# Performance work log

Measured on AMD Instinct MI355X. Metric: run time of the kernel, lower is better.

## Reference

```python
import jax, jax.numpy as jnp
import numpy as np

B, T, F, H, L = 16384, 24, 7, 8, 4
DENSE = [T * H, 1024, 2048, 4]


def setup_inputs() -> dict:
    key = jax.random.key(0)
    d = {"x": jax.random.normal(jax.random.fold_in(key, 0), (B, T, F), jnp.float32)}
    k = 1
    s = 1.0 / np.sqrt(H)  # torch LSTM init bound
    for l in range(L):
        in_dim = F if l == 0 else H
        for name, shape in [("Wih", (4 * H, in_dim)), ("Whh", (4 * H, H)), ("bih", (4 * H,)), ("bhh", (4 * H,))]:
            d[f"{name}{l}"] = jax.random.uniform(jax.random.fold_in(key, k), shape, jnp.float32, -s, s)
            k += 1
    for i in range(1, len(DENSE)):
        si = 1.0 / np.sqrt(DENSE[i - 1])
        d[f"Wd{i}"] = jax.random.uniform(jax.random.fold_in(key, k), (DENSE[i], DENSE[i - 1]), jnp.float32, -si, si)
        k += 1
        d[f"bd{i}"] = jax.random.uniform(jax.random.fold_in(key, k), (DENSE[i],), jnp.float32, -si, si)
        k += 1
    return d


def _lstm_layer(xs, Wih, Whh, b):
    # xs: [T, B, in] -> ys: [T, B, H]; torch gate order i,f,g,o
    Hn = Whh.shape[1]
    h0 = jnp.zeros((xs.shape[1], Hn), xs.dtype)

    def step(carry, xt):
        h, c = carry
        z = xt @ Wih.T + h @ Whh.T + b  # [B, 4H]
        i, f, g, o = jnp.split(z, 4, axis=-1)
        c = jax.nn.sigmoid(f) * c + jax.nn.sigmoid(i) * jnp.tanh(g)
        h = jax.nn.sigmoid(o) * jnp.tanh(c)
        return (h, c), h

    (_, _), ys = jax.lax.scan(step, (h0, h0), xs)
    return ys


def _forward(x, lstm_params, dense_params):
    xs = jnp.transpose(x, (1, 0, 2))  # [T, B, F]
    for (Wih, Whh, bih, bhh) in lstm_params:
        xs = _lstm_layer(xs, Wih, Whh, bih + bhh)
    out = jnp.transpose(xs, (1, 0, 2)).reshape(x.shape[0], T * H)  # [B, 192]
    (W1, b1), (W2, b2), (W3, b3) = dense_params
    out = jax.nn.relu(out @ W1.T + b1)
    out = jax.nn.relu(out @ W2.T + b2)
    return out @ W3.T + b3  # [B, num_classes]


def reference(x, Wih0, Whh0, bih0, bhh0, Wih1, Whh1, bih1, bhh1, Wih2, Whh2, bih2, bhh2, Wih3, Whh3, bih3, bhh3, Wd1, bd1, Wd2, bd2, Wd3, bd3):
    lstm_params = [(Wih0, Whh0, bih0, bhh0), (Wih1, Whh1, bih1, bhh1), (Wih2, Whh2, bih2, bhh2), (Wih3, Whh3, bih3, bhh3)]
    dense_params = [(Wd1, bd1), (Wd2, bd2), (Wd3, bd3)]
    return _forward(x, lstm_params, dense_params)
```

## Files before the change

### kernel.cpp

```cpp
#include <hip/hip_runtime.h>
#include <hip/hip_bf16.h>

typedef __attribute__((ext_vector_type(4))) float f32x4;
typedef __attribute__((ext_vector_type(16))) float f32x16;
typedef __attribute__((ext_vector_type(2))) float f32x2;
typedef __attribute__((ext_vector_type(8))) short bf16x8;

__device__ __forceinline__ ushort f2bf(float f) {
    union { float f; uint u; } v; v.f = f;
    uint u = v.u;
    return (ushort)((u + 0x7fffu + ((u >> 16) & 1u)) >> 16);
}
__device__ __forceinline__ float sigm(float x) {
    return __builtin_amdgcn_rcpf(1.0f + __builtin_amdgcn_exp2f(x * -1.442695040888963f));
}
__device__ __forceinline__ float tanh_(float x) {
    return 2.0f * __builtin_amdgcn_rcpf(1.0f + __builtin_amdgcn_exp2f(x * -2.885390081777927f)) - 1.0f;
}
__device__ __forceinline__ uint pk2(float a, float b) {
    uint r; asm("v_cvt_pk_bf16_f32 %0, %1, %2" : "=v"(r) : "v"(a), "v"(b)); return r;
}
__device__ __forceinline__ bf16x8 pk8(f32x4 lo, f32x4 hi) {
    union { bf16x8 v; uint u[4]; } r;
    r.u[0] = pk2(lo[0], lo[1]); r.u[1] = pk2(lo[2], lo[3]);
    r.u[2] = pk2(hi[0], hi[1]); r.u[3] = pk2(hi[2], hi[3]);
    return r.v;
}

typedef const __attribute__((address_space(1))) unsigned int ga_u32;
typedef __attribute__((address_space(3))) unsigned int lds_u32;
__device__ __forceinline__ void g2l16(const void* g, void* l) {
    __builtin_amdgcn_global_load_lds((ga_u32*)(unsigned long long)g,
                                     (lds_u32*)(unsigned int)(unsigned long long)l,
                                     16, 0, 0);
}

struct LstmW {
    const float* wih[4];
    const float* whh[4];
    const float* bih[4];
    const float* bhh[4];
};

__device__ __forceinline__ void gates8p(const f32x2 w01[8], const f32x2 w23[8],
                                        const float xv8[8], f32x2& a01, f32x2& a23) {
#pragma unroll
    for (int k = 0; k < 8; ++k) {
        f32x2 xv = {xv8[k], xv8[k]};
        a01 += w01[k] * xv;
        a23 += w23[k] * xv;
    }
}
__device__ __forceinline__ void cellup(f32x2 a01, f32x2 a23, float& h, float& c) {
    c = sigm(a01.y) * c + sigm(a01.x) * tanh_(a23.x);
    h = sigm(a23.y) * tanh_(c);
}
__device__ __forceinline__ void ld8(const float* p, float v[8]) {
    float4 a = *(const float4*)p;
    float4 b = *(const float4*)(p + 4);
    v[0] = a.x; v[1] = a.y; v[2] = a.z; v[3] = a.w;
    v[4] = b.x; v[5] = b.y; v[6] = b.z; v[7] = b.w;
}

__global__ __launch_bounds__(256) void pre_kernel(const float* __restrict__ x, LstmW p,
                                                  const float* __restrict__ W1,
                                                  const float* __restrict__ b1,
                                                  const float* __restrict__ W2,
                                                  ushort* __restrict__ W2b,
                                                  const float* __restrict__ b3,
                                                  float* __restrict__ out,
                                                  ushort* __restrict__ H1) {
    const int tid = threadIdx.x;
    if (blockIdx.x >= 512) {
        const int tg = (blockIdx.x - 512) * 256 + tid;
        if (tg < 16384) {
            float4 bv = {b3[0], b3[1], b3[2], b3[3]};
            ((float4*)out)[tg] = bv;
        }
#pragma unroll
        for (int s = 0; s < 4; ++s) {
            int i = tg + s * 131072;
            float4 v = ((const float4*)W2)[i];
            ushort4 r; r.x = f2bf(v.x); r.y = f2bf(v.y); r.z = f2bf(v.z); r.w = f2bf(v.w);
            ((ushort4*)W2b)[i] = r;
        }
        return;
    }

    __shared__ float xs[32 * 168];
    __shared__ float hb[32 * 200];

    const int e0 = blockIdx.x * 32;
    {
        const float4* s = (const float4*)(x + (size_t)e0 * 168);
        float4* d = (float4*)xs;
        for (int i = tid; i < 1344; i += 256) d[i] = s[i];
    }
    __syncthreads();

    const int el = tid >> 3, j = tid & 7;
    float* hr = hb + el * 200;
    const float* xr = xs + el * 168;

    f32x2 wx01[8], wx23[8], wh01[8], wh23[8], b01, b23;

    {
        const float* Wih = p.wih[0];
        const float* Whh = p.whh[0];
#pragma unroll
        for (int k = 0; k < 7; ++k) {
            wx01[k] = {Wih[(0 + j) * 7 + k], Wih[(8 + j) * 7 + k]};
            wx23[k] = {Wih[(16 + j) * 7 + k], Wih[(24 + j) * 7 + k]};
        }
#pragma unroll
        for (int k = 0; k < 8; ++k) {
            wh01[k] = {Whh[(0 + j) * 8 + k], Whh[(8 + j) * 8 + k]};
            wh23[k] = {Whh[(16 + j) * 8 + k], Whh[(24 + j) * 8 + k]};
        }
        b01 = {p.bih[0][j] + p.bhh[0][j], p.bih[0][8 + j] + p.bhh[0][8 + j]};
        b23 = {p.bih[0][16 + j] + p.bhh[0][16 + j], p.bih[0][24 + j] + p.bhh[0][24 + j]};

        float h = 0.f, c = 0.f;
        {
            f32x2 a01 = b01, a23 = b23;
#pragma unroll
            for (int k = 0; k < 7; ++k) {
                f32x2 xv = {xr[k], xr[k]};
                a01 += wx01[k] * xv; a23 += wx23[k] * xv;
            }
            cellup(a01, a23, h, c);
            hr[j] = h;
        }
        for (int t = 1; t < 24; ++t) {
            f32x2 a01 = b01, a23 = b23;
#pragma unroll
            for (int k = 0; k < 7; ++k) {
                f32x2 xv = {xr[t * 7 + k], xr[t * 7 + k]};
                a01 += wx01[k] * xv; a23 += wx23[k] * xv;
            }
            float hp[8]; ld8(&hr[(t - 1) * 8], hp);
            gates8p(wh01, wh23, hp, a01, a23);
            cellup(a01, a23, h, c);
            hr[t * 8 + j] = h;
        }
    }

#pragma unroll
    for (int l = 1; l < 4; ++l) {
        const float* Wih = p.wih[l];
        const float* Whh = p.whh[l];
#pragma unroll
        for (int k = 0; k < 8; ++k) {
            wx01[k] = {Wih[(0 + j) * 8 + k], Wih[(8 + j) * 8 + k]};
            wx23[k] = {Wih[(16 + j) * 8 + k], Wih[(24 + j) * 8 + k]};
            wh01[k] = {Whh[(0 + j) * 8 + k], Whh[(8 + j) * 8 + k]};
            wh23[k] = {Whh[(16 + j) * 8 + k], Whh[(24 + j) * 8 + k]};
        }
        b01 = {p.bih[l][j] + p.bhh[l][j], p.bih[l][8 + j] + p.bhh[l][8 + j]};
        b23 = {p.bih[l][16 + j] + p.bhh[l][16 + j], p.bih[l][24 + j] + p.bhh[l][24 + j]};

        float h = 0.f, c = 0.f;
        {
            float xin[8]; ld8(&hr[0], xin);
            f32x2 a01 = b01, a23 = b23;
            gates8p(wx01, wx23, xin, a01, a23);
            cellup(a01, a23, h, c);
            hr[j] = h;
        }
        for (int t = 1; t < 24; ++t) {
            float xin[8]; ld8(&hr[t * 8], xin);
            float hp[8];  ld8(&hr[(t - 1) * 8], hp);
            f32x2 a01 = b01, a23 = b23;
            gates8p(wx01, wx23, xin, a01, a23);
            gates8p(wh01, wh23, hp, a01, a23);
            cellup(a01, a23, h, c);
            hr[t * 8 + j] = h;
        }
    }

    __syncthreads();
    {
        const int lane = tid & 63;
        const int wv = tid >> 6;
        const int l15 = lane & 15, kq = lane >> 4;
        const int nw0 = wv * 256;

        bf16x8 abf[2][6];
#pragma unroll
        for (int mf = 0; mf < 2; ++mf)
#pragma unroll
            for (int ks = 0; ks < 6; ++ks) {
                const float* ap = hb + (mf * 16 + l15) * 200 + ks * 32 + kq * 8;
                f32x4 lo = *(const f32x4*)ap;
                f32x4 hi = *(const f32x4*)(ap + 4);
                abf[mf][ks] = pk8(lo, hi);
            }
#pragma unroll
        for (int nf = 0; nf < 16; ++nf) {
            const int col = nw0 + nf * 16 + l15;
            const float* wrow = W1 + (size_t)col * 192;
            bf16x8 bbf[6];
#pragma unroll
            for (int ks = 0; ks < 6; ++ks) {
                f32x4 lo = *(const f32x4*)(wrow + ks * 32 + kq * 8);
                f32x4 hi = *(const f32x4*)(wrow + ks * 32 + kq * 8 + 4);
                bbf[ks] = pk8(lo, hi);
            }
            f32x4 a0 = {0.f, 0.f, 0.f, 0.f}, a1 = {0.f, 0.f, 0.f, 0.f};
#pragma unroll
            for (int ks = 0; ks < 6; ++ks) {
                a0 = __builtin_amdgcn_mfma_f32_16x16x32_bf16(abf[0][ks], bbf[ks], a0, 0, 0, 0);
                a1 = __builtin_amdgcn_mfma_f32_16x16x32_bf16(abf[1][ks], bbf[ks], a1, 0, 0, 0);
            }
            const float bv = b1[col];
#pragma unroll
            for (int r = 0; r < 4; ++r) {
                H1[(size_t)(e0 + kq * 4 + r) * 1024 + col]      = f2bf(fmaxf(a0[r] + bv, 0.f));
                H1[(size_t)(e0 + 16 + kq * 4 + r) * 1024 + col] = f2bf(fmaxf(a1[r] + bv, 0.f));
            }
        }
    }
}

template <int OFFB>
__device__ __forceinline__ bf16x8 dsr(unsigned a) {
    bf16x8 r;
    asm volatile("ds_read_b128 %0, %1 offset:%2"
                 : "=v"(r) : "v"(a), "i"(OFFB));
    return r;
}
template <int QA, int QB, int KS>
__device__ __forceinline__ void mma_sub(f32x4 acc[8][4], const bf16x8 afr[8],
                                        const bf16x8 br[4]) {
#pragma unroll
    for (int mi = 0; mi < 4; ++mi)
#pragma unroll
        for (int ni = 0; ni < 2; ++ni)
            acc[QA * 4 + mi][QB * 2 + ni] = __builtin_amdgcn_mfma_f32_16x16x32_bf16(
                afr[mi * 2 + KS], br[ni * 2 + KS], acc[QA * 4 + mi][QB * 2 + ni],
                0, 0, 0);
}

#define SBAR()  __builtin_amdgcn_s_barrier()
#define SCHED0() __builtin_amdgcn_sched_barrier(0)
#define LGKM(N) do { asm volatile("s_waitcnt lgkmcnt(" #N ")"); SCHED0(); } while (0)
#define VMC(N)  do { asm volatile("s_waitcnt vmcnt(" #N ")" ::: "memory"); } while (0)
#define PRIO1() __builtin_amdgcn_s_setprio(1)
#define PRIO0() do { __builtin_amdgcn_s_setprio(0); SCHED0(); } while (0)

__global__ __launch_bounds__(512) void gemm2_kernel(const ushort* __restrict__ A,
                                                    const ushort* __restrict__ W,
                                                    const float* __restrict__ bias,
                                                    const float* __restrict__ W3,
                                                    float* __restrict__ outf) {
    __shared__ alignas(16) ushort smem[65536];
    __shared__ alignas(16) float w3s[1040];

    const int tid = threadIdx.x;
    const int wg = ((int)blockIdx.x & 7) * 64 + ((int)blockIdx.x >> 3);
    const int m0 = (wg >> 3) << 8;
    const int n0 = (wg & 7) << 8;

    const int lane = tid & 63;
    const int wv = tid >> 6;

    const int lrow = tid >> 3;
    const int lc8 = ((tid & 7) ^ (lrow & 7)) << 3;
    const ushort* Ag = A + (size_t)(m0 + lrow) * 1024 + lc8;
    const ushort* Bg = W + (size_t)(n0 + lrow) * 1024 + lc8;
    ushort* const sA0 = smem;
    ushort* const sB0 = smem + 16384;
    ushort* const sA1 = smem + 32768;
    ushort* const sB1 = smem + 49152;
    const int srow64 = (wv << 3) * 64;

    const int l15 = lane & 15, kq = lane >> 4, r7 = l15 & 7;
    const int wM = wv >> 2, wN = wv & 3;
    const unsigned sbase = (unsigned)(unsigned long long)&smem[0];
    const unsigned pc0B = (unsigned)((kq ^ r7) << 4);
    const unsigned pc1B = pc0B ^ 64u;
    const unsigned aRowB = (unsigned)((wM * 128 + l15) * 128);
    const unsigned bRowB = (unsigned)((wN * 64 + l15) * 128);
    const unsigned aA0p0 = sbase + aRowB + pc0B;
    const unsigned aA0p1 = sbase + aRowB + pc1B;
    const unsigned aA1p0 = aA0p0 + 65536u;
    const unsigned aA1p1 = aA0p1 + 65536u;
    const unsigned bB0p0 = sbase + 32768u + bRowB + pc0B;
    const unsigned bB0p1 = sbase + 32768u + bRowB + pc1B;
    const unsigned bB1p0 = bB0p0 + 65536u;
    const unsigned bB1p1 = bB0p1 + 65536u;

    auto stA = [&](int buf, int h, int kt) {
        ushort* b = buf ? sA1 : sA0;
#pragma unroll
        for (int c = 0; c < 2; ++c)
            g2l16(Ag + (size_t)(h * 128 + c * 64) * 1024 + kt * 64,
                  b + (h * 128 + c * 64) * 64 + srow64);
    };
    auto stB = [&](int buf, int h, int kt) {
        ushort* b = buf ? sB1 : sB0;
#pragma unroll
        for (int c = 0; c < 2; ++c)
            g2l16(Bg + (size_t)(h * 128 + c * 64) * 1024 + kt * 64,
                  b + (h * 128 + c * 64) * 64 + srow64);
    };

    f32x4 acc[8][4];
#pragma unroll
    for (int i = 0; i < 8; ++i)
#pragma unroll
        for (int j = 0; j < 4; ++j)
#pragma unroll
            for (int r = 0; r < 4; ++r) acc[i][j][r] = 0.f;

#pragma unroll
    for (int i = 0; i < 2; ++i) {
        int idx = tid + i * 512;
        w3s[(idx >> 8) * 260 + (idx & 255)] = W3[(size_t)(idx >> 8) * 2048 + n0 + (idx & 255)];
    }
    float bias4[4];
#pragma unroll
    for (int ni = 0; ni < 4; ++ni) bias4[ni] = bias[n0 + wN * 64 + ni * 16 + l15];

    stA(0, 0, 0); stA(0, 1, 0); stB(0, 0, 0); stB(0, 1, 0);
    stB(1, 0, 1); stB(1, 1, 1); stA(1, 0, 1);
    asm volatile("s_waitcnt lgkmcnt(0)");
    VMC(6);
    SBAR(); SCHED0();

    bf16x8 afr[8], b0r[4], b1r[4];
    afr[0] = dsr<0>(aA0p0);    afr[2] = dsr<2048>(aA0p0);
    afr[4] = dsr<4096>(aA0p0); afr[6] = dsr<6144>(aA0p0);
    b0r[0] = dsr<0>(bB0p0);    b0r[2] = dsr<2048>(bB0p0);

#pragma unroll 1
    for (int it = 0; it < 8; ++it) {
        const int k1 = 2 * it + 1, k2 = 2 * it + 2, k3 = 2 * it + 3;
        const bool nl = (it < 7);
        SBAR(); SCHED0();
        afr[1] = dsr<0>(aA0p1);    afr[3] = dsr<2048>(aA0p1);
        afr[5] = dsr<4096>(aA0p1); afr[7] = dsr<6144>(aA0p1);
        b0r[1] = dsr<0>(bB0p1);    b0r[3] = dsr<2048>(bB0p1);
        stA(1, 1, k1);
        LGKM(6); PRIO1(); mma_sub<0, 0, 0>(acc, afr, b0r); PRIO0();
        b1r[0] = dsr<4096>(bB0p0); b1r[2] = dsr<6144>(bB0p0);
        LGKM(2); PRIO1(); mma_sub<0, 0, 1>(acc, afr, b0r); PRIO0();
        SBAR(); SCHED0();
        b1r[1] = dsr<4096>(bB0p1); b1r[3] = dsr<6144>(bB0p1);
        LGKM(2); PRIO1(); mma_sub<0, 1, 0>(acc, afr, b1r); PRIO0();
        afr[0] = dsr<8192>(aA0p0);  afr[2] = dsr<10240>(aA0p0);
        afr[4] = dsr<12288>(aA0p0); afr[6] = dsr<14336>(aA0p0);
        LGKM(4); PRIO1(); mma_sub<0, 1, 1>(acc, afr, b1r); PRIO0();
        SBAR(); SCHED0();
        afr[1] = dsr<8192>(aA0p1);  afr[3] = dsr<10240>(aA0p1);
        afr[5] = dsr<12288>(aA0p1); afr[7] = dsr<14336>(aA0p1);
        if (nl) stB(0, 0, k2);
        LGKM(4); PRIO1(); mma_sub<1, 1, 0>(acc, afr, b1r); PRIO0();
        LGKM(0); PRIO1(); mma_sub<1, 1, 1>(acc, afr, b1r); PRIO0();
        if (nl) { VMC(2); } else { VMC(0); }
        SBAR(); SCHED0();
        if (nl) { stB(0, 1, k2); stA(0, 0, k2); }
        PRIO1(); mma_sub<1, 0, 0>(acc, afr, b0r); PRIO0();
        afr[0] = dsr<8192>(aA1p0);  afr[2] = dsr<10240>(aA1p0);
        afr[4] = dsr<12288>(aA1p0); afr[6] = dsr<14336>(aA1p0);
        b0r[0] = dsr<0>(bB1p0);     b0r[2] = dsr<2048>(bB1p0);
        PRIO1(); mma_sub<1, 0, 1>(acc, afr, b0r); PRIO0();
        SBAR(); SCHED0();
        afr[1] = dsr<8192>(aA1p1);  afr[3] = dsr<10240>(aA1p1);
        afr[5] = dsr<12288>(aA1p1); afr[7] = dsr<14336>(aA1p1);
        b0r[1] = dsr<0>(bB1p1);     b0r[3] = dsr<2048>(bB1p1);
        if (nl) stA(0, 1, k2);
        LGKM(6); PRIO1(); mma_sub<1, 0, 0>(acc, afr, b0r); PRIO0();
        b1r[0] = dsr<4096>(bB1p0); b1r[2] = dsr<6144>(bB1p0);
        LGKM(2); PRIO1(); mma_sub<1, 0, 1>(acc, afr, b0r); PRIO0();
        SBAR(); SCHED0();
        b1r[1] = dsr<4096>(bB1p1); b1r[3] = dsr<6144>(bB1p1);
        LGKM(2); PRIO1(); mma_sub<1, 1, 0>(acc, afr, b1r); PRIO0();
        afr[0] = dsr<0>(aA1p0);    afr[2] = dsr<2048>(aA1p0);
        afr[4] = dsr<4096>(aA1p0); afr[6] = dsr<6144>(aA1p0);
        LGKM(4); PRIO1(); mma_sub<1, 1, 1>(acc, afr, b1r); PRIO0();
        SBAR(); SCHED0();
        afr[1] = dsr<0>(aA1p1);    afr[3] = dsr<2048>(aA1p1);
        afr[5] = dsr<4096>(aA1p1); afr[7] = dsr<6144>(aA1p1);
        if (nl) stB(1, 0, k3);
        LGKM(4); PRIO1(); mma_sub<0, 1, 0>(acc, afr, b1r); PRIO0();
        LGKM(0); PRIO1(); mma_sub<0, 1, 1>(acc, afr, b1r); PRIO0();
        if (nl) { VMC(2); }
        SBAR(); SCHED0();
        if (nl) { stB(1, 1, k3); stA(1, 0, k3); }
        PRIO1(); mma_sub<0, 0, 0>(acc, afr, b0r); PRIO0();
        if (nl) {
            afr[0] = dsr<0>(aA0p0);    afr[2] = dsr<2048>(aA0p0);
            afr[4] = dsr<4096>(aA0p0); afr[6] = dsr<6144>(aA0p0);
            b0r[0] = dsr<0>(bB0p0);    b0r[2] = dsr<2048>(bB0p0);
        }
        PRIO1(); mma_sub<0, 0, 1>(acc, afr, b0r); PRIO0();
    }

    float* Cs = (float*)smem;
    const int drow = tid >> 3;
    const int j8 = tid & 7;
    __syncthreads();
#pragma unroll
    for (int s = 0; s < 4; ++s) {
        if (wM == (s >> 1)) {
            const int mb = (s & 1) * 4;
#pragma unroll
            for (int mi = 0; mi < 4; ++mi)
#pragma unroll
                for (int ni = 0; ni < 4; ++ni) {
                    f32x4 v = acc[mb + mi][ni];
                    const int cbase = (mi * 16 + kq * 4) * 260 + wN * 64 + ni * 16 + l15;
#pragma unroll
                    for (int r = 0; r < 4; ++r)
                        Cs[cbase + r * 260] = fmaxf(v[r] + bias4[ni], 0.f);
                }
        }
        __syncthreads();
        {
            const float* crow = &Cs[drow * 260 + j8 * 4];
            f32x4 pp = {0.f, 0.f, 0.f, 0.f};
#pragma unroll
            for (int k = 0; k < 8; ++k) {
                f32x4 cv = *(const f32x4*)(crow + k * 32);
#pragma unroll
                for (int q = 0; q < 4; ++q) {
                    f32x4 wv4 = *(const f32x4*)(&w3s[q * 260 + j8 * 4 + k * 32]);
                    pp[q] += cv[0] * wv4[0] + cv[1] * wv4[1] + cv[2] * wv4[2] + cv[3] * wv4[3];
                }
            }
#pragma unroll
            for (int m = 1; m < 8; m <<= 1) {
#pragma unroll
                for (int q = 0; q < 4; ++q) pp[q] += __shfl_xor(pp[q], m);
            }
            const float pv = (j8 == 0) ? pp[0] : (j8 == 1) ? pp[1]
                           : (j8 == 2) ? pp[2] : pp[3];
            if (j8 < 4)
                atomicAdd(&outf[(size_t)(m0 + s * 64 + drow) * 4 + j8], pv);
        }
        __syncthreads();
    }
}

extern "C" void kernel_launch(void* const* d_in, const int* in_sizes, int n_in,
                              void* d_out, int out_size, void* d_ws, size_t ws_size,
                              hipStream_t stream) {
    const float* x = (const float*)d_in[0];
    LstmW w;
    for (int l = 0; l < 4; ++l) {
        w.wih[l] = (const float*)d_in[1 + 4 * l];
        w.whh[l] = (const float*)d_in[2 + 4 * l];
        w.bih[l] = (const float*)d_in[3 + 4 * l];
        w.bhh[l] = (const float*)d_in[4 + 4 * l];
    }
    const float* Wd1 = (const float*)d_in[17];
    const float* bd1 = (const float*)d_in[18];
    const float* Wd2 = (const float*)d_in[19];
    const float* bd2 = (const float*)d_in[20];
    const float* Wd3 = (const float*)d_in[21];
    const float* bd3 = (const float*)d_in[22];
    float* out = (float*)d_out;

    ushort* H1  = (ushort*)((char*)d_ws + 6291456);
    ushort* W2b = (ushort*)((char*)d_ws + 40239104);

    pre_kernel<<<1024, 256, 0, stream>>>(x, w, Wd1, bd1, Wd2, W2b, bd3, out, H1);
    gemm2_kernel<<<512, 512, 0, stream>>>(H1, W2b, bd2, Wd3, out);
}
```

Baseline: 225.7 us.

## Prefetch next-step input projection and read LSTM inputs directly from global

The LDS staging buffer for x and its block barrier are removed. Each thread now loads its element's inputs straight from global memory. Every LSTM layer is software-pipelined so the input-to-gate product for step t+1 is computed while step t's recurrent update runs, taking it off the serial recurrence path. This frees about 21KB of shared memory per block, which may allow higher occupancy. In exchange it adds scattered, partly redundant global loads, since 8 lanes read the same x values, plus an extra wasted projection on the last step.

Measured after the change: 232.1 us. 2.8% more time.

```diff
diff --git a/kernel.cpp b/kernel.cpp
--- a/kernel.cpp
+++ b/kernel.cpp
@@ -87,20 +87,12 @@
         return;
     }
 
-    __shared__ float xs[32 * 168];
     __shared__ float hb[32 * 200];
 
     const int e0 = blockIdx.x * 32;
-    {
-        const float4* s = (const float4*)(x + (size_t)e0 * 168);
-        float4* d = (float4*)xs;
-        for (int i = tid; i < 1344; i += 256) d[i] = s[i];
-    }
-    __syncthreads();
-
     const int el = tid >> 3, j = tid & 7;
     float* hr = hb + el * 200;
-    const float* xr = xs + el * 168;
+    const float* xg = x + (size_t)(e0 + el) * 168;
 
     f32x2 wx01[8], wx23[8], wh01[8], wh23[8], b01, b23;
 
@@ -121,27 +113,37 @@
         b23 = {p.bih[0][16 + j] + p.bhh[0][16 + j], p.bih[0][24 + j] + p.bhh[0][24 + j]};
 
         float h = 0.f, c = 0.f;
+        f32x2 zx01 = b01, zx23 = b23;
         {
-            f32x2 a01 = b01, a23 = b23;
+            float xn[7];
+#pragma unroll
+            for (int k = 0; k < 7; ++k) xn[k] = xg[k];
 #pragma unroll
             for (int k = 0; k < 7; ++k) {
-                f32x2 xv = {xr[k], xr[k]};
-                a01 += wx01[k] * xv; a23 += wx23[k] * xv;
-            }
-            cellup(a01, a23, h, c);
-            hr[j] = h;
-        }
-        for (int t = 1; t < 24; ++t) {
-            f32x2 a01 = b01, a23 = b23;
-#pragma unroll
-            for (int k = 0; k < 7; ++k) {
-                f32x2 xv = {xr[t * 7 + k], xr[t * 7 + k]};
-                a01 += wx01[k] * xv; a23 += wx23[k] * xv;
-            }
-            float hp[8]; ld8(&hr[(t - 1) * 8], hp);
-            gates8p(wh01, wh23, hp, a01, a23);
+                f32x2 xv = {xn[k], xn[k]};
+                zx01 += wx01[k] * xv; zx23 += wx23[k] * xv;
+            }
+        }
+        for (int t = 0; t < 24; ++t) {
+            float hp[8];
+            if (t > 0) ld8(&hr[(t - 1) * 8], hp);
+            const int tn = (t < 23) ? t + 1 : 23;
+            f32x2 nz01 = b01, nz23 = b23;
+            {
+                float xm[7];
+#pragma unroll
+                for (int k = 0; k < 7; ++k) xm[k] = xg[tn * 7 + k];
+#pragma unroll
+                for (int k = 0; k < 7; ++k) {
+                    f32x2 xv = {xm[k], xm[k]};
+                    nz01 += wx01[k] * xv; nz23 += wx23[k] * xv;
+                }
+            }
+            f32x2 a01 = zx01, a23 = zx23;
+            if (t > 0) gates8p(wh01, wh23, hp, a01, a23);
             cellup(a01, a23, h, c);
             hr[t * 8 + j] = h;
+            zx01 = nz01; zx23 = nz23;
         }
     }
 
@@ -160,21 +162,23 @@
         b23 = {p.bih[l][16 + j] + p.bhh[l][16 + j], p.bih[l][24 + j] + p.bhh[l][24 + j]};
 
         float h = 0.f, c = 0.f;
+        f32x2 zx01 = b01, zx23 = b23;
         {
-            float xin[8]; ld8(&hr[0], xin);
-            f32x2 a01 = b01, a23 = b23;
-            gates8p(wx01, wx23, xin, a01, a23);
-            cellup(a01, a23, h, c);
-            hr[j] = h;
-        }
-        for (int t = 1; t < 24; ++t) {
-            float xin[8]; ld8(&hr[t * 8], xin);
-            float hp[8];  ld8(&hr[(t - 1) * 8], hp);
-            f32x2 a01 = b01, a23 = b23;
-            gates8p(wx01, wx23, xin, a01, a23);
-            gates8p(wh01, wh23, hp, a01, a23);
+            float xn[8]; ld8(&hr[0], xn);
+            gates8p(wx01, wx23, xn, zx01, zx23);
+        }
+        for (int t = 0; t < 24; ++t) {
+            float hp[8];
+            if (t > 0) ld8(&hr[(t - 1) * 8], hp);
+            const int tn = (t < 23) ? t + 1 : 23;
+            float xm[8]; ld8(&hr[tn * 8], xm);
+            f32x2 nz01 = b01, nz23 = b23;
+            gates8p(wx01, wx23, xm, nz01, nz23);
+            f32x2 a01 = zx01, a23 = zx23;
+            if (t > 0) gates8p(wh01, wh23, hp, a01, a23);
             cellup(a01, a23, h, c);
             hr[t * 8 + j] = h;
+            zx01 = nz01; zx23 = nz23;
         }
     }
 
```
